# Kernel optimization log

Measured on AMD Instinct MI355X. Metric: run time of the kernel, lower is better.

Reference implementation:

```python
import jax, jax.numpy as jnp
import numpy as np

B, M, N = 32, 512, 512
XD = YD = 512   # x_size, y_size
S = 512         # shared_size
H = 512         # hidden_size
MAXD = 11       # max relative distance


def _lin(k, i, o):
    lim = float(np.sqrt(6.0 / (i + o)))  # xavier_uniform, gain=1
    return jax.random.uniform(k, (i, o), jnp.float32, -lim, lim)


def setup_inputs() -> dict:
    key = jax.random.key(0)
    ks = jax.random.split(key, 16)
    inp = {
        'prem': jax.random.normal(ks[0], (B, M, YD), jnp.float32),
        'hypo': jax.random.normal(ks[1], (B, N, XD), jnp.float32),
        'prem_mask': jnp.ones((B, M), dtype=bool),
        'hypo_mask': jnp.ones((B, N), dtype=bool),
        # projections
        'Wpx': _lin(ks[2], XD, S), 'bpx': jnp.zeros((S,), jnp.float32),
        'Wpy': _lin(ks[3], YD, S), 'bpy': jnp.zeros((S,), jnp.float32),
        # relative-distance bias embedding (2*max_dist+1, squeezed to scalar)
        'dist_embed': jax.random.normal(ks[4], (2 * MAXD + 1,), jnp.float32),
        # self-attention DeepDot MLP: S -> H -> H
        'Ws1': _lin(ks[5], S, H), 'bs1': jnp.zeros((H,), jnp.float32),
        'Ws2': _lin(ks[6], H, H), 'bs2': jnp.zeros((H,), jnp.float32),
        # cross-attention DeepDot MLP: 2S -> H -> H
        'Wa1': _lin(ks[7], 2 * S, H), 'ba1': jnp.zeros((H,), jnp.float32),
        'Wa2': _lin(ks[8], H, H), 'ba2': jnp.zeros((H,), jnp.float32),
        # compare layer: 4S -> H -> H
        'Wc1': _lin(ks[9], 4 * S, H), 'bc1': jnp.zeros((H,), jnp.float32),
        'Wc2': _lin(ks[10], H, H), 'bc2': jnp.zeros((H,), jnp.float32),
        # aggregate layer: 2H -> H -> H
        'Wg1': _lin(ks[11], 2 * H, H), 'bg1': jnp.zeros((H,), jnp.float32),
        'Wg2': _lin(ks[12], H, H), 'bg2': jnp.zeros((H,), jnp.float32),
    }
    return inp


def _mlp2(x, W1, b1, W2, b2):
    # Linear -> ReLU -> Linear -> ReLU (dropout=0.0)
    h = jax.nn.relu(x @ W1 + b1)
    return jax.nn.relu(h @ W2 + b2)


def _rel_bias(size, dist_embed):
    v = jnp.arange(size)
    d = jnp.clip(v[None, :] - v[:, None], -MAXD, MAXD) + MAXD  # [size,size]
    return dist_embed[d]


def _masked_softmax(t, mask):
    # mask True = valid; broadcast over query dim
    return jax.nn.softmax(jnp.where(mask, t, -jnp.inf), axis=-1)


def reference(prem, hypo, prem_mask, hypo_mask,
              Wpx, bpx, Wpy, bpy, dist_embed,
              Ws1, bs1, Ws2, bs2,
              Wa1, ba1, Wa2, ba2,
              Wc1, bc1, Wc2, bc2,
              Wg1, bg1, Wg2, bg2):
    hypo_p = hypo @ Wpx + bpx   # [B,N,S]
    prem_p = prem @ Wpy + bpy   # [B,M,S]

    # self attention (DeepDot: shared MLP on q and k, then qk^T)
    fp = _mlp2(prem_p, Ws1, bs1, Ws2, bs2)
    fh = _mlp2(hypo_p, Ws1, bs1, Ws2, bs2)
    p_scores = jnp.einsum('bmh,bnh->bmn', fp, fp) + _rel_bias(prem_p.shape[1], dist_embed)[None]
    h_scores = jnp.einsum('bmh,bnh->bmn', fh, fh) + _rel_bias(hypo_p.shape[1], dist_embed)[None]

    p_att = _masked_softmax(p_scores, prem_mask[:, None, :])
    h_att = _masked_softmax(h_scores, hypo_mask[:, None, :])
    prem_ctx = jnp.einsum('bmn,bnd->bmd', p_att, prem_p)
    hypo_ctx = jnp.einsum('bmn,bnd->bmd', h_att, hypo_p)

    prem2 = jnp.concatenate([prem_p, prem_ctx], axis=-1)  # [B,M,2S]
    hypo2 = jnp.concatenate([hypo_p, hypo_ctx], axis=-1)  # [B,N,2S]

    # cross attention
    gp = _mlp2(prem2, Wa1, ba1, Wa2, ba2)
    gh = _mlp2(hypo2, Wa1, ba1, Wa2, ba2)
    sim = jnp.einsum('bmh,bnh->bmn', gp, gh)  # [B,M,N]
    p2h = _masked_softmax(sim, hypo_mask[:, None, :])
    h2p = _masked_softmax(jnp.swapaxes(sim, 1, 2), prem_mask[:, None, :])
    attended_hypo = jnp.einsum('bmn,bnd->bmd', p2h, hypo2)  # [B,M,2S]
    attended_prem = jnp.einsum('bnm,bmd->bnd', h2p, prem2)  # [B,N,2S]

    prem_cmp = _mlp2(jnp.concatenate([prem2, attended_hypo], -1), Wc1, bc1, Wc2, bc2)
    hypo_cmp = _mlp2(jnp.concatenate([hypo2, attended_prem], -1), Wc1, bc1, Wc2, bc2)

    prem_cmp = (prem_cmp * prem_mask[..., None].astype(prem_cmp.dtype)).sum(axis=1)  # [B,H]
    hypo_cmp = (hypo_cmp * hypo_mask[..., None].astype(hypo_cmp.dtype)).sum(axis=1)  # [B,H]

    return _mlp2(jnp.concatenate([prem_cmp, hypo_cmp], -1), Wg1, bg1, Wg2, bg2)
```

## Files before the change

kernel.cpp:

```cpp
#include <hip/hip_runtime.h>
#include <hip/hip_bf16.h>


typedef __bf16 bf16x8 __attribute__((ext_vector_type(8)));
typedef float floatx16 __attribute__((ext_vector_type(16)));

__device__ __forceinline__ unsigned short f32_to_bf16(float f) {
    unsigned int u = __float_as_uint(f);
    unsigned int r = (u + 0x7FFFu + ((u >> 16) & 1u)) >> 16;
    return (unsigned short)r;
}
__device__ __forceinline__ float bf16_to_f32(unsigned short h) {
    return __uint_as_float(((unsigned int)h) << 16);
}

struct TW {
    const float* src[8];
    unsigned short* dst[8];
    int K[8];
};
__global__ __launch_bounds__(256) void transpose_all_kernel(TW tw) {
    const int z = blockIdx.z;
    const int K = tw.K[z];
    const int k0 = blockIdx.y * 32;
    if (k0 >= K) return;
    const float* W = tw.src[z];
    unsigned short* Wt = tw.dst[z];
    __shared__ unsigned short tile[32][33];
    int n0 = blockIdx.x * 32;
    int tx = threadIdx.x & 31, ty = threadIdx.x >> 5;
    #pragma unroll
    for (int i = 0; i < 4; ++i) {
        int ky = ty + i * 8;
        tile[ky][tx] = f32_to_bf16(W[(long long)(k0 + ky) * 512 + n0 + tx]);
    }
    __syncthreads();
    #pragma unroll
    for (int i = 0; i < 4; ++i) {
        int ny = ty + i * 8;
        Wt[(long long)(n0 + ny) * K + k0 + tx] = tile[tx][ny];
    }
}

template <bool BT, bool AF32>
__global__ __launch_bounds__(256, 4) void gemm_kernel(
    const void* __restrict__ Av, const void* __restrict__ A2v, int lda, long long strideA,
    const unsigned short* __restrict__ Bw, int ldb, long long strideB, int bxor,
    const unsigned short* __restrict__ B2, const float* __restrict__ bias2, int Msplit,
    float* __restrict__ C32, unsigned short* __restrict__ Cb, int ldc, long long strideC,
    const float* __restrict__ bias, int relu, int M, int N, int K,
    float* __restrict__ csum, int swz) {
    constexpr int BBYTES = BT ? 8192 : (32 * 264);
    constexpr int BUF = 8192 + BBYTES;
    __shared__ alignas(16) char smem[2 * BUF];

    const int t = threadIdx.x;
    const int lane = t & 63;
    const int wave = t >> 6;
    const int wm = (wave >> 1) * 64;
    const int wn = (wave & 1) * 64;
    const int ln = lane & 31;
    const int h = lane >> 5;

    int bx = blockIdx.x, by = blockIdx.y, bz = blockIdx.z;
    if (swz == 1) {
        int Nt = gridDim.x, Mt = gridDim.y;
        int L = by * Nt + bx;
        int x = L & 7, s = L >> 3;
        by = x * (Mt >> 3) + s / Nt;
        bx = s % Nt;
    } else if (swz == 2) {
        int Nt = gridDim.x, Mt = gridDim.y;
        int L = (bz * Mt + by) * Nt + bx;
        int x = L & 7, s = L >> 3;
        int mg = x * ((Mt * (int)gridDim.z) >> 3) + s / Nt;
        bx = s % Nt;
        by = mg % Mt;
        bz = mg / Mt;
    }
    const int m0 = by * 128;
    const int n0 = bx * 128;
    const int bzB = (bz + bxor) & ((int)gridDim.z - 1);

    const unsigned short* B = Bw;
    const float* biasp = bias;
    long long mA = m0;
    if (Msplit && m0 >= Msplit) {
        if (B2) B = B2;
        if (bias2) biasp = bias2;
        if (A2v) { Av = A2v; mA = m0 - Msplit; }
    }

    const float* aptrF = nullptr;
    const unsigned short* aptrH = nullptr;
    if constexpr (AF32)
        aptrF = (const float*)Av + (long long)bz * strideA +
                (mA + (t >> 1)) * (long long)lda + (t & 1) * 16;
    else
        aptrH = (const unsigned short*)Av + (long long)bz * strideA +
                (mA + (t >> 1)) * (long long)lda + (t & 1) * 16;
    const unsigned short* bptr;
    if (BT)
        bptr = B + (long long)bzB * strideB +
               (long long)(n0 + (t >> 1)) * ldb + (t & 1) * 16;
    else
        bptr = B + (long long)bzB * strideB +
               (long long)(t >> 4) * ldb + n0 + (t & 15) * 8;
    const long long bstep = BT ? 8 : 16 * (long long)ldb;

    const int aoff = ((t & 1) * 256 + (t >> 1)) * 16;
    const int boff = BT ? (8192 + ((t & 1) * 256 + (t >> 1)) * 16)
                        : (8192 + (t >> 4) * 264 + (t & 15) * 16);
    const int boff2 = BT ? 2048 : 16 * 264;

    floatx16 acc[2][2];
    #pragma unroll
    for (int im = 0; im < 2; ++im)
        #pragma unroll
        for (int in = 0; in < 2; ++in)
            acc[im][in] = (floatx16)(0.f);

    uint4 va0, va1, vb0, vb1;
    float4 fa0, fa1, fa2, fa3;

    auto loadA = [&]() {
        if constexpr (AF32) {
            fa0 = *(const float4*)(aptrF);
            fa1 = *(const float4*)(aptrF + 4);
            fa2 = *(const float4*)(aptrF + 8);
            fa3 = *(const float4*)(aptrF + 12);
            aptrF += 32;
        } else {
            va0 = *(const uint4*)(aptrH);
            va1 = *(const uint4*)(aptrH + 8);
            aptrH += 32;
        }
    };
    auto loadB = [&]() {
        vb0 = *(const uint4*)(bptr);
        vb1 = *(const uint4*)(bptr + bstep);
        bptr += BT ? 32 : 32 * (long long)ldb;
    };
    auto commit = [&](char* buf) {
        if constexpr (AF32) {
            union { uint4 q; unsigned short u[8]; } c0, c1;
            c0.u[0] = f32_to_bf16(fa0.x); c0.u[1] = f32_to_bf16(fa0.y);
            c0.u[2] = f32_to_bf16(fa0.z); c0.u[3] = f32_to_bf16(fa0.w);
            c0.u[4] = f32_to_bf16(fa1.x); c0.u[5] = f32_to_bf16(fa1.y);
            c0.u[6] = f32_to_bf16(fa1.z); c0.u[7] = f32_to_bf16(fa1.w);
            c1.u[0] = f32_to_bf16(fa2.x); c1.u[1] = f32_to_bf16(fa2.y);
            c1.u[2] = f32_to_bf16(fa2.z); c1.u[3] = f32_to_bf16(fa2.w);
            c1.u[4] = f32_to_bf16(fa3.x); c1.u[5] = f32_to_bf16(fa3.y);
            c1.u[6] = f32_to_bf16(fa3.z); c1.u[7] = f32_to_bf16(fa3.w);
            *(uint4*)(buf + aoff) = c0.q;
            *(uint4*)(buf + aoff + 2048) = c1.q;
        } else {
            *(uint4*)(buf + aoff) = va0;
            *(uint4*)(buf + aoff + 2048) = va1;
        }
        *(uint4*)(buf + boff) = vb0;
        *(uint4*)(buf + boff + boff2) = vb1;
    };

    loadA(); loadB();
    commit(smem);
    loadA(); loadB();
    __syncthreads();

    int p = 0;
    for (int k0 = 0; k0 < K; k0 += 32) {
        const char* base = smem + p * BUF;
        #pragma unroll
        for (int s = 0; s < 2; ++s) {
            bf16x8 a[2], b[2];
            #pragma unroll
            for (int im = 0; im < 2; ++im)
                a[im] = *(const bf16x8*)(base + ((s * 2 + h) * 128 + wm + im * 32 + ln) * 16);
            if (BT) {
                #pragma unroll
                for (int in = 0; in < 2; ++in)
                    b[in] = *(const bf16x8*)(base + 8192 +
                                             ((s * 2 + h) * 128 + wn + in * 32 + ln) * 16);
            } else {
                #pragma unroll
                for (int in = 0; in < 2; ++in) {
                    union { bf16x8 v; unsigned short u[8]; } u;
                    #pragma unroll
                    for (int j = 0; j < 8; ++j)
                        u.u[j] = *(const unsigned short*)(base + 8192 +
                                 (s * 16 + h * 8 + j) * 264 + (wn + in * 32 + ln) * 2);
                    b[in] = u.v;
                }
            }
            #pragma unroll
            for (int im = 0; im < 2; ++im)
                #pragma unroll
                for (int in = 0; in < 2; ++in)
                    acc[im][in] = __builtin_amdgcn_mfma_f32_32x32x16_bf16(
                        a[im], b[in], acc[im][in], 0, 0, 0);
        }

        if (k0 + 32 < K) {
            commit(smem + (p ^ 1) * BUF);
            if (k0 + 64 < K) { loadA(); loadB(); }
            __syncthreads();
            p ^= 1;
        }
    }

    if (csum) {
        const int bidx = m0 >> 9;
        const long long cbase = (long long)(bidx & 31) * 1024 + (bidx >> 5) * 512;
        #pragma unroll
        for (int in = 0; in < 2; ++in) {
            int n = n0 + wn + in * 32 + ln;
            float bn = biasp ? biasp[n] : 0.f;
            float s = 0.f;
            #pragma unroll
            for (int im = 0; im < 2; ++im)
                #pragma unroll
                for (int r = 0; r < 16; ++r) {
                    float v = acc[im][in][r] + bn;
                    if (relu) v = fmaxf(v, 0.f);
                    s += v;
                }
            s += __shfl_xor(s, 32);
            if (lane < 32) atomicAdd(&csum[cbase + n], s);
        }
        return;
    }

    float* C32b = C32 ? C32 + (long long)bz * strideC : nullptr;
    unsigned short* Cbb = Cb ? Cb + (long long)bz * strideC : nullptr;
    #pragma unroll
    for (int im = 0; im < 2; ++im) {
        #pragma unroll
        for (int in = 0; in < 2; ++in) {
            int n = n0 + wn + in * 32 + ln;
            float bn = biasp ? biasp[n] : 0.f;
            #pragma unroll
            for (int r = 0; r < 16; ++r) {
                int m = m0 + wm + im * 32 + (r & 3) + 8 * (r >> 2) + 4 * h;
                float v = acc[im][in][r] + bn;
                if (relu) v = fmaxf(v, 0.f);
                long long off = (long long)m * ldc + n;
                if (C32b) C32b[off] = v;
                if (Cbb) Cbb[off] = f32_to_bf16(v);
            }
        }
    }
}

__global__ __launch_bounds__(256) void softmax_kernel(const float* S,
                                                      unsigned short* P,
                                                      const float* de, int rel) {
    const int row = blockIdx.x;
    const int b = blockIdx.y;
    const long long baseS = ((long long)b * 512 + row) * 512;
    const long long baseP = ((long long)b * 512 + row) * 1024;
    const int t = threadIdx.x;
    const int lane = t & 63, wv = t >> 6;
    __shared__ float redmax[4], redsum[4];

    float v[2];
    float mx = -1e30f;
    #pragma unroll
    for (int i = 0; i < 2; ++i) {
        int c = t + i * 256;
        float x = S[baseS + c];
        if (rel) {
            int d = c - row;
            d = min(11, max(-11, d));
            x += de[d + 11];
        }
        v[i] = x;
        mx = fmaxf(mx, x);
    }
    #pragma unroll
    for (int o = 32; o > 0; o >>= 1) mx = fmaxf(mx, __shfl_down(mx, o));
    if (lane == 0) redmax[wv] = mx;
    __syncthreads();
    mx = fmaxf(fmaxf(redmax[0], redmax[1]), fmaxf(redmax[2], redmax[3]));

    float s = 0.f;
    #pragma unroll
    for (int i = 0; i < 2; ++i) { v[i] = __expf(v[i] - mx); s += v[i]; }
    #pragma unroll
    for (int o = 32; o > 0; o >>= 1) s += __shfl_down(s, o);
    if (lane == 0) redsum[wv] = s;
    __syncthreads();
    s = redsum[0] + redsum[1] + redsum[2] + redsum[3];
    float inv = 1.f / s;
    #pragma unroll
    for (int i = 0; i < 2; ++i) P[baseP + t + i * 256] = f32_to_bf16(v[i] * inv);
}

__global__ __launch_bounds__(512) void mlp_agg_kernel(const float* __restrict__ X,
                                                      const float* __restrict__ W,
                                                      const float* __restrict__ bias,
                                                      float* __restrict__ out,
                                                      int K, int N, int relu) {
    const int b = blockIdx.y;
    const int nl = threadIdx.x & 63;
    const int n = blockIdx.x * 64 + nl;
    const int ks = threadIdx.x >> 6;
    const int kchunk = K >> 3;
    const float* Xb = X + (long long)b * K;
    const int k0 = ks * kchunk;
    float s = 0.f;
    #pragma unroll 8
    for (int k = k0; k < k0 + kchunk; ++k)
        s += Xb[k] * W[(long long)k * N + n];
    __shared__ float red[8][64];
    red[ks][nl] = s;
    __syncthreads();
    if (threadIdx.x < 64) {
        float t = 0.f;
        #pragma unroll
        for (int i = 0; i < 8; ++i) t += red[i][threadIdx.x];
        t += bias[n];
        if (relu) t = fmaxf(t, 0.f);
        out[(long long)b * N + n] = t;
    }
}

static void gemm(hipStream_t st, bool bt, bool af32,
                 const void* A, const void* A2, int lda, long long sA,
                 const void* B, int ldb, long long sB, int bxor,
                 const void* B2, const float* bias2, int Msplit,
                 float* C32, void* Cb, int ldc, long long sC,
                 const float* bias, int relu, int M, int N, int K, int batch,
                 float* csum = nullptr) {
    dim3 g(N / 128, M / 128, batch), blk(256);
    int swz = 0;
    if (batch == 1 && (M / 128) % 8 == 0) swz = 1;
    else if (batch > 1 && ((M / 128) * batch) % 8 == 0) swz = 2;
    if (bt) {
        if (af32)
            gemm_kernel<true, true><<<g, blk, 0, st>>>(
                A, A2, lda, sA, (const unsigned short*)B, ldb, sB, bxor,
                (const unsigned short*)B2, bias2, Msplit,
                C32, (unsigned short*)Cb, ldc, sC, bias, relu, M, N, K, csum, swz);
        else
            gemm_kernel<true, false><<<g, blk, 0, st>>>(
                A, A2, lda, sA, (const unsigned short*)B, ldb, sB, bxor,
                (const unsigned short*)B2, bias2, Msplit,
                C32, (unsigned short*)Cb, ldc, sC, bias, relu, M, N, K, csum, swz);
    } else {
        gemm_kernel<false, false><<<g, blk, 0, st>>>(
            A, A2, lda, sA, (const unsigned short*)B, ldb, sB, bxor,
            (const unsigned short*)B2, bias2, Msplit,
            C32, (unsigned short*)Cb, ldc, sC, bias, relu, M, N, K, csum, swz);
    }
}

extern "C" void kernel_launch(void* const* d_in, const int* in_sizes, int n_in,
                              void* d_out, int out_size, void* d_ws, size_t ws_size,
                              hipStream_t stream) {
    const int B = 32, SEQ = 512;
    const int MT = B * SEQ;
    const int M2 = 2 * MT;

    const float* prem = (const float*)d_in[0];
    const float* hypo = (const float*)d_in[1];
    const float* Wpx = (const float*)d_in[4];  const float* bpx = (const float*)d_in[5];
    const float* Wpy = (const float*)d_in[6];  const float* bpy = (const float*)d_in[7];
    const float* de  = (const float*)d_in[8];
    const float* Ws1 = (const float*)d_in[9];  const float* bs1 = (const float*)d_in[10];
    const float* Ws2 = (const float*)d_in[11]; const float* bs2 = (const float*)d_in[12];
    const float* Wa1 = (const float*)d_in[13]; const float* ba1 = (const float*)d_in[14];
    const float* Wa2 = (const float*)d_in[15]; const float* ba2 = (const float*)d_in[16];
    const float* Wc1 = (const float*)d_in[17]; const float* bc1 = (const float*)d_in[18];
    const float* Wc2 = (const float*)d_in[19]; const float* bc2 = (const float*)d_in[20];
    const float* Wg1 = (const float*)d_in[21]; const float* bg1 = (const float*)d_in[22];
    const float* Wg2 = (const float*)d_in[23]; const float* bg2 = (const float*)d_in[24];

    char* p = (char*)d_ws;
    auto alloc = [&](size_t bytes) { char* r = p; p += (bytes + 255) & ~(size_t)255; return r; };
    unsigned short* prem_bf = (unsigned short*)alloc((size_t)MT * 512 * 2);
    unsigned short* hypo_bf = (unsigned short*)alloc((size_t)MT * 512 * 2);
    unsigned short* premcat = (unsigned short*)alloc((size_t)MT * 2048 * 2);
    unsigned short* hypocat = (unsigned short*)alloc((size_t)MT * 2048 * 2);
    float* scores = (float*)alloc((size_t)64 * SEQ * SEQ * 4);
    unsigned short* h1 = (unsigned short*)scores;
    unsigned short* att = (unsigned short*)scores;
    unsigned short* Wpx_t = (unsigned short*)alloc(512 * 512 * 2);
    unsigned short* Wpy_t = (unsigned short*)alloc(512 * 512 * 2);
    unsigned short* Ws1_t = (unsigned short*)alloc(512 * 512 * 2);
    unsigned short* Ws2_t = (unsigned short*)alloc(512 * 512 * 2);
    unsigned short* Wa1_t = (unsigned short*)alloc(512 * 1024 * 2);
    unsigned short* Wa2_t = (unsigned short*)alloc(512 * 512 * 2);
    unsigned short* Wc1_t = (unsigned short*)alloc(512 * 2048 * 2);
    unsigned short* Wc2_t = (unsigned short*)alloc(512 * 512 * 2);
    float* agg  = (float*)alloc(32 * 1024 * 4);
    float* aggh = (float*)alloc(32 * 512 * 4);
    (void)hypo_bf; (void)hypocat;

    const long long sBM = (long long)SEQ * SEQ;
    const long long sAtt = (long long)SEQ * 1024;
    const long long sCat = (long long)SEQ * 2048;

    {
        TW tw;
        tw.src[0] = Wpy; tw.dst[0] = Wpy_t; tw.K[0] = 512;
        tw.src[1] = Wpx; tw.dst[1] = Wpx_t; tw.K[1] = 512;
        tw.src[2] = Ws1; tw.dst[2] = Ws1_t; tw.K[2] = 512;
        tw.src[3] = Ws2; tw.dst[3] = Ws2_t; tw.K[3] = 512;
        tw.src[4] = Wa1; tw.dst[4] = Wa1_t; tw.K[4] = 1024;
        tw.src[5] = Wa2; tw.dst[5] = Wa2_t; tw.K[5] = 512;
        tw.src[6] = Wc1; tw.dst[6] = Wc1_t; tw.K[6] = 2048;
        tw.src[7] = Wc2; tw.dst[7] = Wc2_t; tw.K[7] = 512;
        transpose_all_kernel<<<dim3(16, 64, 8), 256, 0, stream>>>(tw);
        hipMemsetAsync(agg, 0, 32 * 1024 * sizeof(float), stream);
    }

    gemm(stream, true, true, prem, hypo, 512, 0, Wpy_t, 512, 0, 0,
         Wpx_t, bpx, MT, nullptr, premcat, 2048, 0, bpy, 0, M2, 512, 512, 1);

    gemm(stream, true, false, premcat, nullptr, 2048, 0, Ws1_t, 512, 0, 0,
         nullptr, nullptr, 0, nullptr, h1, 512, 0, bs1, 1, M2, 512, 512, 1);
    gemm(stream, true, false, h1, nullptr, 512, 0, Ws2_t, 512, 0, 0,
         nullptr, nullptr, 0, nullptr, prem_bf, 512, 0, bs2, 1, M2, 512, 512, 1);

    gemm(stream, true, false, prem_bf, nullptr, 512, sBM, prem_bf, 512, sBM, 0,
         nullptr, nullptr, 0, scores, nullptr, 512, sBM, nullptr, 0, 512, 512, 512, 64);
    softmax_kernel<<<dim3(512, 64), 256, 0, stream>>>(scores, att, de, 1);
    gemm(stream, false, false, att, nullptr, 1024, sAtt, premcat, 2048, sCat, 0,
         nullptr, nullptr, 0, nullptr, premcat + 512, 2048, sCat, nullptr, 0, 512, 512, 512, 64);

    gemm(stream, true, false, premcat, nullptr, 2048, 0, Wa1_t, 1024, 0, 0,
         nullptr, nullptr, 0, nullptr, h1, 512, 0, ba1, 1, M2, 512, 1024, 1);
    gemm(stream, true, false, h1, nullptr, 512, 0, Wa2_t, 512, 0, 0,
         nullptr, nullptr, 0, nullptr, prem_bf, 512, 0, ba2, 1, M2, 512, 512, 1);

    gemm(stream, true, false, prem_bf, nullptr, 512, sBM, prem_bf, 512, sBM, 32,
         nullptr, nullptr, 0, scores, nullptr, 512, sBM, nullptr, 0, 512, 512, 512, 64);
    softmax_kernel<<<dim3(512, 64), 256, 0, stream>>>(scores, att, de, 0);
    gemm(stream, false, false, att, nullptr, 1024, sAtt, premcat, 2048, sCat, 32,
         nullptr, nullptr, 0, nullptr, premcat + 1024, 2048, sCat, nullptr, 0, 512, 1024, 512, 64);

    gemm(stream, true, false, premcat, nullptr, 2048, 0, Wc1_t, 2048, 0, 0,
         nullptr, nullptr, 0, nullptr, h1, 512, 0, bc1, 1, M2, 512, 2048, 1);
    gemm(stream, true, false, h1, nullptr, 512, 0, Wc2_t, 512, 0, 0,
         nullptr, nullptr, 0, nullptr, nullptr, 512, 0, bc2, 1, M2, 512, 512, 1, agg);

    mlp_agg_kernel<<<dim3(8, 32), 512, 0, stream>>>(agg, Wg1, bg1, aggh, 1024, 512, 1);
    mlp_agg_kernel<<<dim3(8, 32), 512, 0, stream>>>(aggh, Wg2, bg2, (float*)d_out, 512, 512, 1);
}
```

Before: 648.4 us.

## Add 256x256-tile bf16 GEMM with direct-to-LDS loads for NT GEMMs

Adds a new GEMM kernel that computes 256x256 output tiles with 512 threads. It stages operands through double-buffered 128KB shared memory using global_load_lds, with an XOR swizzle, interleaved partial-tile MFMA phases, setprio, and a grid remap for cache locality. Most weight-projection GEMMs and the score GEMMs move to this kernel, aiming for more data reuse per tile and overlap of loads with MFMA work. The risks are fewer workgroups per GEMM, high register and LDS pressure, and reliance on K being a multiple of 64 and on batch counts being powers of two.

```diff
diff --git a/kernel.cpp b/kernel.cpp
--- a/kernel.cpp
+++ b/kernel.cpp
@@ -4,6 +4,7 @@
 
 typedef __bf16 bf16x8 __attribute__((ext_vector_type(8)));
 typedef float floatx16 __attribute__((ext_vector_type(16)));
+typedef float floatx4 __attribute__((ext_vector_type(4)));
 
 __device__ __forceinline__ unsigned short f32_to_bf16(float f) {
     unsigned int u = __float_as_uint(f);
@@ -13,6 +14,16 @@
 __device__ __forceinline__ float bf16_to_f32(unsigned short h) {
     return __uint_as_float(((unsigned int)h) << 16);
 }
+
+__device__ __forceinline__ void gload16(const void* g, void* l) {
+    __builtin_amdgcn_global_load_lds(
+        (const __attribute__((address_space(1))) unsigned int*)g,
+        (__attribute__((address_space(3))) unsigned int*)l, 16, 0, 0);
+}
+
+#define FENCE_BAR() do { asm volatile("" ::: "memory"); \
+    __builtin_amdgcn_s_barrier(); \
+    asm volatile("" ::: "memory"); } while (0)
 
 struct TW {
     const float* src[8];
@@ -242,6 +253,199 @@
             for (int r = 0; r < 16; ++r) {
                 int m = m0 + wm + im * 32 + (r & 3) + 8 * (r >> 2) + 4 * h;
                 float v = acc[im][in][r] + bn;
+                if (relu) v = fmaxf(v, 0.f);
+                long long off = (long long)m * ldc + n;
+                if (C32b) C32b[off] = v;
+                if (Cbb) Cbb[off] = f32_to_bf16(v);
+            }
+        }
+    }
+}
+
+__global__ __launch_bounds__(512, 2) void gemm256_kernel(
+    const unsigned short* __restrict__ Aw, int lda, long long strideA,
+    const unsigned short* __restrict__ Bw, int ldb, long long strideB, int bxor,
+    float* __restrict__ C32, unsigned short* __restrict__ Cb, int ldc, long long strideC,
+    const float* __restrict__ bias, int relu, int K) {
+    extern __shared__ __align__(16) char smem[];
+
+    const int tid = threadIdx.x;
+    const int lane = tid & 63;
+    const int wave = tid >> 6;
+    const int wr = wave >> 2;
+    const int wc = wave & 3;
+
+    int bx = blockIdx.x, by = blockIdx.y, bz = blockIdx.z;
+    {
+        const int gx = gridDim.x, gy = gridDim.y;
+        const int nwg = gx * gy * (int)gridDim.z;
+        if ((nwg & 7) == 0) {
+            int L = (bz * gy + by) * gx + bx;
+            int flat = (L & 7) * (nwg >> 3) + (L >> 3);
+            bx = flat % gx;
+            int R = flat / gx;
+            by = R % gy;
+            bz = R / gy;
+        }
+    }
+    const int m0 = by * 256;
+    const int n0 = bx * 256;
+    const int bzB = (bz + bxor) & ((int)gridDim.z - 1);
+
+    const int rowT = tid >> 3;
+    const int chS = (tid & 7) ^ (rowT & 7);
+    const long long ldaB = (long long)lda * 2;
+    const long long ldbB = (long long)ldb * 2;
+    const char* aG = (const char*)Aw +
+        ((long long)bz * strideA + (long long)(m0 + rowT) * lda) * 2 + chS * 16;
+    const char* bG = (const char*)Bw +
+        ((long long)bzB * strideB + (long long)(n0 + rowT) * ldb) * 2 + chS * 16;
+    const int dOff = tid * 16;
+
+    auto stA = [&](int tt, int h) {
+        const char* g = aG + (long long)(h * 128) * ldaB + (long long)tt * 128;
+        char* l = smem + (tt & 1) * 65536 + h * 16384 + dOff;
+        gload16(g, l);
+        gload16(g + 64 * ldaB, l + 8192);
+    };
+    auto stB = [&](int tt, int h) {
+        const char* g = bG + (long long)(h * 128) * ldbB + (long long)tt * 128;
+        char* l = smem + (tt & 1) * 65536 + 32768 + h * 16384 + dOff;
+        gload16(g, l);
+        gload16(g + 64 * ldbB, l + 8192);
+    };
+
+    const int l15 = lane & 15;
+    const int lk = lane >> 4;
+    const int swzb = (lane & 7) << 4;
+    const int c0 = (lk * 16) ^ swzb;
+    const int c1 = (64 + lk * 16) ^ swzb;
+    const int arow = (wr * 128 + l15) * 128;
+    const int brow = 32768 + (wc * 64 + l15) * 128;
+
+    floatx4 acc[8][4];
+    #pragma unroll
+    for (int mf = 0; mf < 8; ++mf)
+        #pragma unroll
+        for (int nf = 0; nf < 4; ++nf)
+            acc[mf][nf] = (floatx4)(0.f);
+
+    const int NT = K >> 6;
+
+    stA(0, 0); stA(0, 1); stB(0, 0); stB(0, 1);
+    if (NT > 1) {
+        stB(1, 0); stB(1, 1);
+        asm volatile("s_waitcnt vmcnt(4)" ::: "memory");
+    } else {
+        asm volatile("s_waitcnt vmcnt(0)" ::: "memory");
+    }
+    FENCE_BAR();
+
+    bf16x8 a[4][2], b[4][2];
+    for (int t = 0; t < NT; ++t) {
+        const char* buf = smem + (t & 1) * 65536;
+        const char* aB = buf + arow;
+        const char* bB = buf + brow;
+
+        #pragma unroll
+        for (int mf = 0; mf < 4; ++mf) {
+            a[mf][0] = *(const bf16x8*)(aB + mf * 2048 + c0);
+            a[mf][1] = *(const bf16x8*)(aB + mf * 2048 + c1);
+        }
+        #pragma unroll
+        for (int nf = 0; nf < 2; ++nf) {
+            b[nf][0] = *(const bf16x8*)(bB + nf * 2048 + c0);
+            b[nf][1] = *(const bf16x8*)(bB + nf * 2048 + c1);
+        }
+        if (t + 1 < NT) stA(t + 1, 0);
+        FENCE_BAR();
+        __builtin_amdgcn_s_setprio(1);
+        #pragma unroll
+        for (int mf = 0; mf < 4; ++mf)
+            #pragma unroll
+            for (int nf = 0; nf < 2; ++nf) {
+                acc[mf][nf] = __builtin_amdgcn_mfma_f32_16x16x32_bf16(
+                    a[mf][0], b[nf][0], acc[mf][nf], 0, 0, 0);
+                acc[mf][nf] = __builtin_amdgcn_mfma_f32_16x16x32_bf16(
+                    a[mf][1], b[nf][1], acc[mf][nf], 0, 0, 0);
+            }
+        __builtin_amdgcn_s_setprio(0);
+        FENCE_BAR();
+
+        #pragma unroll
+        for (int nf = 2; nf < 4; ++nf) {
+            b[nf][0] = *(const bf16x8*)(bB + nf * 2048 + c0);
+            b[nf][1] = *(const bf16x8*)(bB + nf * 2048 + c1);
+        }
+        if (t + 1 < NT) stA(t + 1, 1);
+        FENCE_BAR();
+        __builtin_amdgcn_s_setprio(1);
+        #pragma unroll
+        for (int mf = 0; mf < 4; ++mf)
+            #pragma unroll
+            for (int nf = 2; nf < 4; ++nf) {
+                acc[mf][nf] = __builtin_amdgcn_mfma_f32_16x16x32_bf16(
+                    a[mf][0], b[nf][0], acc[mf][nf], 0, 0, 0);
+                acc[mf][nf] = __builtin_amdgcn_mfma_f32_16x16x32_bf16(
+                    a[mf][1], b[nf][1], acc[mf][nf], 0, 0, 0);
+            }
+        __builtin_amdgcn_s_setprio(0);
+        FENCE_BAR();
+
+        #pragma unroll
+        for (int mf = 0; mf < 4; ++mf) {
+            a[mf][0] = *(const bf16x8*)(aB + (4 + mf) * 2048 + c0);
+            a[mf][1] = *(const bf16x8*)(aB + (4 + mf) * 2048 + c1);
+        }
+        if (t + 2 < NT) stB(t + 2, 0);
+        FENCE_BAR();
+        __builtin_amdgcn_s_setprio(1);
+        #pragma unroll
+        for (int mf = 0; mf < 4; ++mf)
+            #pragma unroll
+            for (int nf = 2; nf < 4; ++nf) {
+                acc[4 + mf][nf] = __builtin_amdgcn_mfma_f32_16x16x32_bf16(
+                    a[mf][0], b[nf][0], acc[4 + mf][nf], 0, 0, 0);
+                acc[4 + mf][nf] = __builtin_amdgcn_mfma_f32_16x16x32_bf16(
+                    a[mf][1], b[nf][1], acc[4 + mf][nf], 0, 0, 0);
+            }
+        __builtin_amdgcn_s_setprio(0);
+        FENCE_BAR();
+
+        if (t + 2 < NT) {
+            stB(t + 2, 1);
+            asm volatile("s_waitcnt vmcnt(4)" ::: "memory");
+        } else {
+            asm volatile("s_waitcnt vmcnt(0)" ::: "memory");
+        }
+        FENCE_BAR();
+        __builtin_amdgcn_s_setprio(1);
+        #pragma unroll
+        for (int mf = 0; mf < 4; ++mf)
+            #pragma unroll
+            for (int nf = 0; nf < 2; ++nf) {
+                acc[4 + mf][nf] = __builtin_amdgcn_mfma_f32_16x16x32_bf16(
+                    a[mf][0], b[nf][0], acc[4 + mf][nf], 0, 0, 0);
+                acc[4 + mf][nf] = __builtin_amdgcn_mfma_f32_16x16x32_bf16(
+                    a[mf][1], b[nf][1], acc[4 + mf][nf], 0, 0, 0);
+            }
+        __builtin_amdgcn_s_setprio(0);
+        FENCE_BAR();
+    }
+
+    const int rg = (lane >> 4) * 4;
+    float* C32b = C32 ? C32 + (long long)bz * strideC : nullptr;
+    unsigned short* Cbb = Cb ? Cb + (long long)bz * strideC : nullptr;
+    #pragma unroll
+    for (int nf = 0; nf < 4; ++nf) {
+        const int n = n0 + wc * 64 + nf * 16 + l15;
+        const float bn = bias ? bias[n] : 0.f;
+        #pragma unroll
+        for (int mf = 0; mf < 8; ++mf) {
+            #pragma unroll
+            for (int r = 0; r < 4; ++r) {
+                int m = m0 + wr * 128 + mf * 16 + rg + r;
+                float v = acc[mf][nf][r] + bn;
                 if (relu) v = fmaxf(v, 0.f);
                 long long off = (long long)m * ldc + n;
                 if (C32b) C32b[off] = v;
@@ -354,6 +558,24 @@
     }
 }
 
+static void gemm256(hipStream_t st,
+                    const void* A, int lda, long long sA,
+                    const void* B, int ldb, long long sB, int bxor,
+                    float* C32, void* Cb, int ldc, long long sC,
+                    const float* bias, int relu, int M, int N, int K, int batch) {
+    static bool inited = false;
+    if (!inited) {
+        hipFuncSetAttribute(reinterpret_cast<const void*>(gemm256_kernel),
+                            hipFuncAttributeMaxDynamicSharedMemorySize, 131072);
+        inited = true;
+    }
+    dim3 g(N / 256, M / 256, batch);
+    gemm256_kernel<<<g, 512, 131072, st>>>(
+        (const unsigned short*)A, lda, sA,
+        (const unsigned short*)B, ldb, sB, bxor,
+        C32, (unsigned short*)Cb, ldc, sC, bias, relu, K);
+}
+
 extern "C" void kernel_launch(void* const* d_in, const int* in_sizes, int n_in,
                               void* d_out, int out_size, void* d_ws, size_t ws_size,
                               hipStream_t stream) {
@@ -417,30 +639,30 @@
     gemm(stream, true, true, prem, hypo, 512, 0, Wpy_t, 512, 0, 0,
          Wpx_t, bpx, MT, nullptr, premcat, 2048, 0, bpy, 0, M2, 512, 512, 1);
 
-    gemm(stream, true, false, premcat, nullptr, 2048, 0, Ws1_t, 512, 0, 0,
-         nullptr, nullptr, 0, nullptr, h1, 512, 0, bs1, 1, M2, 512, 512, 1);
-    gemm(stream, true, false, h1, nullptr, 512, 0, Ws2_t, 512, 0, 0,
-         nullptr, nullptr, 0, nullptr, prem_bf, 512, 0, bs2, 1, M2, 512, 512, 1);
-
-    gemm(stream, true, false, prem_bf, nullptr, 512, sBM, prem_bf, 512, sBM, 0,
-         nullptr, nullptr, 0, scores, nullptr, 512, sBM, nullptr, 0, 512, 512, 512, 64);
+    gemm256(stream, premcat, 2048, 0, Ws1_t, 512, 0, 0,
+            nullptr, h1, 512, 0, bs1, 1, M2, 512, 512, 1);
+    gemm256(stream, h1, 512, 0, Ws2_t, 512, 0, 0,
+            nullptr, prem_bf, 512, 0, bs2, 1, M2, 512, 512, 1);
+
+    gemm256(stream, prem_bf, 512, sBM, prem_bf, 512, sBM, 0,
+            scores, nullptr, 512, sBM, nullptr, 0, 512, 512, 512, 64);
     softmax_kernel<<<dim3(512, 64), 256, 0, stream>>>(scores, att, de, 1);
     gemm(stream, false, false, att, nullptr, 1024, sAtt, premcat, 2048, sCat, 0,
          nullptr, nullptr, 0, nullptr, premcat + 512, 2048, sCat, nullptr, 0, 512, 512, 512, 64);
 
-    gemm(stream, true, false, premcat, nullptr, 2048, 0, Wa1_t, 1024, 0, 0,
-         nullptr, nullptr, 0, nullptr, h1, 512, 0, ba1, 1, M2, 512, 1024, 1);
-    gemm(stream, true, false, h1, nullptr, 512, 0, Wa2_t, 512, 0, 0,
-         nullptr, nullptr, 0, nullptr, prem_bf, 512, 0, ba2, 1, M2, 512, 512, 1);
-
-    gemm(stream, true, false, prem_bf, nullptr, 512, sBM, prem_bf, 512, sBM, 32,
-         nullptr, nullptr, 0, scores, nullptr, 512, sBM, nullptr, 0, 512, 512, 512, 64);
+    gemm256(stream, premcat, 2048, 0, Wa1_t, 1024, 0, 0,
+            nullptr, h1, 512, 0, ba1, 1, M2, 512, 1024, 1);
+    gemm256(stream, h1, 512, 0, Wa2_t, 512, 0, 0,
+            nullptr, prem_bf, 512, 0, ba2, 1, M2, 512, 512, 1);
+
+    gemm256(stream, prem_bf, 512, sBM, prem_bf, 512, sBM, 32,
+            scores, nullptr, 512, sBM, nullptr, 0, 512, 512, 512, 64);
     softmax_kernel<<<dim3(512, 64), 256, 0, stream>>>(scores, att, de, 0);
     gemm(stream, false, false, att, nullptr, 1024, sAtt, premcat, 2048, sCat, 32,
          nullptr, nullptr, 0, nullptr, premcat + 1024, 2048, sCat, nullptr, 0, 512, 1024, 512, 64);
 
-    gemm(stream, true, false, premcat, nullptr, 2048, 0, Wc1_t, 2048, 0, 0,
-         nullptr, nullptr, 0, nullptr, h1, 512, 0, bc1, 1, M2, 512, 2048, 1);
+    gemm256(stream, premcat, 2048, 0, Wc1_t, 2048, 0, 0,
+            nullptr, h1, 512, 0, bc1, 1, M2, 512, 2048, 1);
     gemm(stream, true, false, h1, nullptr, 512, 0, Wc2_t, 512, 0, 0,
          nullptr, nullptr, 0, nullptr, nullptr, 512, 0, bc2, 1, M2, 512, 512, 1, agg);
 
```

Measured after the change: 658.2 us. Within noise of the previous version (+1.5%).
